# Kernel tuning notes

Hardware: AMD Instinct MI355X
Metric: run time of the kernel (lower is better)

## Reference

```python
import jax, jax.numpy as jnp
import numpy as np

N = 256    # num_nodes = 2*K*R
K = 16     # num_cluster (after reflection pairing)
R = 8      # ratio = size of each original cluster
IN = 32
OUT = 32
BS = 32


def setup_inputs() -> dict:
    key = jax.random.key(0)
    k1, k2, k3, k4 = jax.random.split(key, 4)
    x = jax.random.normal(k1, (BS, N, IN), dtype=jnp.float32)
    w_diag = jax.random.uniform(k2, (IN * OUT, K), dtype=jnp.float32)           # torch.rand
    w_off = jax.random.uniform(k3, (IN * OUT, K, 2 * K), dtype=jnp.float32)     # torch.rand
    stdv = 1.0 / np.sqrt(OUT)
    b1 = jax.random.uniform(k4, (OUT,), minval=-stdv, maxval=stdv, dtype=jnp.float32)
    perm = np.random.default_rng(0).permutation(N)   # flatten_ids of shuffled clusters
    permute_ids = jnp.asarray(perm, dtype=jnp.int32)
    inv_permute = jnp.asarray(np.argsort(perm), dtype=jnp.int32)
    return {"x": x, "w_diag": w_diag, "w_off": w_off, "b1": b1,
            "permute_ids": permute_ids, "inv_permute": inv_permute}


def _build_W(w_diag, w_off):
    # Faithful to: kron(tie_weights(w_off), ones(R,R))/N + kron(diag_embed(repeat_interleave(w_diag,2)), eye(R))
    C = w_diag.shape[0]            # in*out channels
    width = 2 * K
    # tie_weights: interleave original rows with pair-swapped-column rows
    swap = np.arange(width).reshape(-1, 2)[:, ::-1].reshape(-1)      # [1,0,3,2,...]
    tied = jnp.stack([w_off, w_off[:, :, swap]], axis=2).reshape(C, width, width)
    # kron with ones(R,R) == repeat each entry R times along both node axes
    W3 = jnp.repeat(jnp.repeat(tied, R, axis=1), R, axis=2) / N      # (C, N, N)
    # kron(diag_embed(.), eye(R)) == add per-node diagonal, constant within cluster
    wd_full = jnp.repeat(jnp.repeat(w_diag, 2, axis=1), R, axis=1)   # (C, N)
    di = jnp.arange(N)
    W3 = W3.at[:, di, di].add(wd_full)
    # rearrange '(o i) j k -> (o j) (i k)'
    return W3.reshape(OUT, IN, N, N).transpose(0, 2, 1, 3).reshape(OUT * N, IN * N)


def reference(x, w_diag, w_off, b1, permute_ids, inv_permute):
    W = _build_W(w_diag, w_off)                       # (OUT*N, IN*N)
    xp = x[:, permute_ids, :]                         # (BS, N, IN) permuted
    xp = xp.transpose(0, 2, 1).reshape(BS, IN * N)    # feature-major flatten
    out = xp @ W.T                                    # (BS, OUT*N)
    out = out.reshape(BS, OUT, N).transpose(0, 2, 1)  # (BS, N, OUT)
    out = out[:, inv_permute, :] + b1[None, None, :]
    return out
```

## Files before the change

kernel.cpp:

```cpp
#include <hip/hip_runtime.h>

#define N_   256
#define IN_  32
#define OUT_ 32
#define BS_  32

__global__ __launch_bounds__(256) void k_yz(const float* __restrict__ x,
                                            const int* __restrict__ perm,
                                            const float* __restrict__ w_off,
                                            float* __restrict__ ws_z) {
    const int t = threadIdx.x;
    const int b = blockIdx.x;
    const int o  = b & 31;
    const int sg = b >> 5;
    const int u  = t & 15;
    const int i4 = (t >> 4) & 7;
    const int sh = t >> 7;

    __shared__ int   perm_s[256];
    __shared__ float y_lds[4 * 32 * 32];
    __shared__ float part[128][8];

    perm_s[t] = perm[t];

    float4 wv[4][8];
    const float* wbase = w_off + ((o * 32 + i4 * 4) * 16 + u) * 32;
#pragma unroll
    for (int di = 0; di < 4; ++di)
#pragma unroll
        for (int q4 = 0; q4 < 8; ++q4)
            wv[di][q4] = *(const float4*)(wbase + di * 512 + q4 * 4);

    __syncthreads();

    {
        const int i  = t & 31;
        const int qb = t >> 5;
#pragma unroll
        for (int sl = 0; sl < 4; ++sl) {
            const float* xs = x + (sg * 4 + sl) * (N_ * IN_);
#pragma unroll
            for (int k = 0; k < 4; ++k) {
                const int q = qb * 4 + k;
                float sum = 0.f;
#pragma unroll
                for (int j = 0; j < 8; ++j)
                    sum += xs[perm_s[8 * q + j] * IN_ + i];
                y_lds[sl * 1024 + q * 32 + i] = sum;
            }
        }
    }
    __syncthreads();

#define WEL(di, qq) (((const float*)&wv[di][(qq) >> 2])[(qq) & 3])

    float accs[2][2];
#pragma unroll
    for (int dsi = 0; dsi < 2; ++dsi) {
        const float* yb = y_lds + (sh * 2 + dsi) * 1024 + i4 * 4;
        float a0 = 0.f, a1 = 0.f;
#pragma unroll
        for (int q = 0; q < 32; ++q) {
            const float4 yv = *(const float4*)(yb + q * 32);
            const int q1 = q ^ 1;
            a0 += WEL(0, q)  * yv.x + WEL(1, q)  * yv.y + WEL(2, q)  * yv.z + WEL(3, q)  * yv.w;
            a1 += WEL(0, q1) * yv.x + WEL(1, q1) * yv.y + WEL(2, q1) * yv.z + WEL(3, q1) * yv.w;
        }
        accs[dsi][0] = a0;
        accs[dsi][1] = a1;
    }
#undef WEL

#pragma unroll
    for (int dsi = 0; dsi < 2; ++dsi)
#pragma unroll
        for (int p = 0; p < 2; ++p) {
            const int slot = ((sh * 2 + dsi) * 16 + u) * 2 + p;
            part[slot][i4] = accs[dsi][p];
        }
    __syncthreads();

    if (t < 128) {
        float sum = 0.f;
#pragma unroll
        for (int j = 0; j < 8; ++j) sum += part[t][j];
        const int s_local = t >> 5;
        const int uu = (t >> 1) & 15;
        const int pp = t & 1;
        const int s = sg * 4 + s_local;
        ws_z[((s * 32 + o) * 16 + uu) * 2 + pp] = sum * (1.0f / 256.0f);
    }
}

__global__ __launch_bounds__(256) void k_out(const float* __restrict__ x,
                                             const int* __restrict__ perm,
                                             const float* __restrict__ w_diag,
                                             const float* __restrict__ b1,
                                             const float* __restrict__ ws_z,
                                             float* __restrict__ out) {
    const int t = threadIdx.x;
    const int b = blockIdx.x;
    const int s = b >> 3;
    const int ac = b & 7;

    __shared__ float xrow[32 * 32];
    __shared__ float wdt[2][32 * 36];
    __shared__ float z_lds[1024];
    __shared__ int perm_lds[32];

    if (t < 32) perm_lds[t] = perm[ac * 32 + t];

    ((float4*)z_lds)[t] = ((const float4*)(ws_z + s * 1024))[t];

    {
        const int o = t >> 3;
        const int ii = (t & 7) * 4;
#pragma unroll
        for (int uu = 0; uu < 2; ++uu)
#pragma unroll
            for (int d = 0; d < 4; ++d)
                wdt[uu][o * 36 + ii + d] = w_diag[(o * 32 + ii + d) * 16 + ac * 2 + uu];
    }
    {
        const int r = t >> 3;
        const int col = (t & 7) * 4;
        const int rowp = perm[ac * 32 + r];
        const float4 v = *(const float4*)(x + (s * N_ + rowp) * IN_ + col);
        *(float4*)&xrow[r * 32 + col] = v;
    }
    __syncthreads();

    const int o = t & 31;
    const int rg = t >> 5;
    const int u_sel = rg >> 2;
    const int p = (rg >> 1) & 1;
    const int u = ac * 2 + u_sel;

    float4 wreg[8];
#pragma unroll
    for (int ii = 0; ii < 8; ++ii)
        wreg[ii] = *(const float4*)&wdt[u_sel][o * 36 + ii * 4];

    const float base = b1[o] + z_lds[(o * 16 + u) * 2 + p];

#pragma unroll
    for (int dr = 0; dr < 4; ++dr) {
        const int r = rg * 4 + dr;
        const float4* xr = (const float4*)&xrow[r * 32];
        float acc = base;
#pragma unroll
        for (int ii = 0; ii < 8; ++ii) {
            const float4 xv = xr[ii];
            const float4 wv = wreg[ii];
            acc += xv.x * wv.x + xv.y * wv.y + xv.z * wv.z + xv.w * wv.w;
        }
        out[(s * N_ + perm_lds[r]) * OUT_ + o] = acc;
    }
}

extern "C" void kernel_launch(void* const* d_in, const int* in_sizes, int n_in,
                              void* d_out, int out_size, void* d_ws, size_t ws_size,
                              hipStream_t stream) {
    const float* x      = (const float*)d_in[0];
    const float* w_diag = (const float*)d_in[1];
    const float* w_off  = (const float*)d_in[2];
    const float* b1     = (const float*)d_in[3];
    const int*   perm   = (const int*)d_in[4];

    float* out = (float*)d_out;
    float* ws_z = (float*)d_ws;

    k_yz<<<256, 256, 0, stream>>>(x, perm, w_off, ws_z);
    k_out<<<256, 256, 0, stream>>>(x, perm, w_diag, b1, ws_z, out);
}
```

Before: 75.51 us.

## Fuse cluster-sum and output kernels into one per-sample, per-cluster-block kernel

Merges the two kernels into a single kernel where each block owns one sample and a block of 32 nodes. It computes the cluster sums and the off-diagonal contribution locally instead of staging z through workspace memory. This removes a kernel launch and the global round trip, but each block now recomputes the cluster sums for its sample (8x redundancy). It also loads w_off tiles for only its two clusters, in two sequential register loads.

```diff
diff --git a/kernel.cpp b/kernel.cpp
--- a/kernel.cpp
+++ b/kernel.cpp
@@ -5,26 +5,31 @@
 #define OUT_ 32
 #define BS_  32
 
-__global__ __launch_bounds__(256) void k_yz(const float* __restrict__ x,
-                                            const int* __restrict__ perm,
-                                            const float* __restrict__ w_off,
-                                            float* __restrict__ ws_z) {
+__global__ __launch_bounds__(256) void k_fused(const float* __restrict__ x,
+                                               const int* __restrict__ perm,
+                                               const float* __restrict__ w_diag,
+                                               const float* __restrict__ w_off,
+                                               const float* __restrict__ b1,
+                                               float* __restrict__ out) {
     const int t = threadIdx.x;
     const int b = blockIdx.x;
-    const int o  = b & 31;
-    const int sg = b >> 5;
-    const int u  = t & 15;
-    const int i4 = (t >> 4) & 7;
-    const int sh = t >> 7;
+    const int s  = b >> 3;
+    const int ac = b & 7;
 
     __shared__ int   perm_s[256];
-    __shared__ float y_lds[4 * 32 * 32];
-    __shared__ float part[128][8];
+    __shared__ float y_lds[1024];
+    __shared__ float part[128][9];
+    __shared__ float z_lds[128];
+    __shared__ float xrow[1024];
+    __shared__ float wdt[2][32 * 36];
 
     perm_s[t] = perm[t];
 
+    const int o  = t & 31;
+    const int i4 = t >> 5;
+
+    const float* wbase = w_off + ((o * 32 + i4 * 4) * 16 + 2 * ac) * 32;
     float4 wv[4][8];
-    const float* wbase = w_off + ((o * 32 + i4 * 4) * 16 + u) * 32;
 #pragma unroll
     for (int di = 0; di < 4; ++di)
 #pragma unroll
@@ -34,30 +39,46 @@
     __syncthreads();
 
     {
-        const int i  = t & 31;
-        const int qb = t >> 5;
+        const float* xs = x + s * (N_ * IN_);
 #pragma unroll
-        for (int sl = 0; sl < 4; ++sl) {
-            const float* xs = x + (sg * 4 + sl) * (N_ * IN_);
+        for (int k = 0; k < 4; ++k) {
+            const int q = i4 * 4 + k;
+            float sum = 0.f;
 #pragma unroll
-            for (int k = 0; k < 4; ++k) {
-                const int q = qb * 4 + k;
-                float sum = 0.f;
+            for (int j = 0; j < 8; ++j)
+                sum += xs[perm_s[8 * q + j] * IN_ + o];
+            y_lds[q * 32 + o] = sum;
+        }
+    }
+    {
+        const int r = t >> 3;
+        const int col = (t & 7) * 4;
+        const float4 v = *(const float4*)(x + (s * N_ + perm_s[ac * 32 + r]) * IN_ + col);
+        *(float4*)&xrow[r * 32 + col] = v;
+    }
+    {
+        const int oo = t >> 3;
+        const int ii = (t & 7) * 4;
 #pragma unroll
-                for (int j = 0; j < 8; ++j)
-                    sum += xs[perm_s[8 * q + j] * IN_ + i];
-                y_lds[sl * 1024 + q * 32 + i] = sum;
-            }
-        }
+        for (int uu = 0; uu < 2; ++uu)
+#pragma unroll
+            for (int d = 0; d < 4; ++d)
+                wdt[uu][oo * 36 + ii + d] = w_diag[(oo * 32 + ii + d) * 16 + ac * 2 + uu];
     }
     __syncthreads();
 
 #define WEL(di, qq) (((const float*)&wv[di][(qq) >> 2])[(qq) & 3])
 
-    float accs[2][2];
+    const float* yb = y_lds + i4 * 4;
 #pragma unroll
-    for (int dsi = 0; dsi < 2; ++dsi) {
-        const float* yb = y_lds + (sh * 2 + dsi) * 1024 + i4 * 4;
+    for (int u_l = 0; u_l < 2; ++u_l) {
+        if (u_l == 1) {
+#pragma unroll
+            for (int di = 0; di < 4; ++di)
+#pragma unroll
+                for (int q4 = 0; q4 < 8; ++q4)
+                    wv[di][q4] = *(const float4*)(wbase + di * 512 + 32 + q4 * 4);
+        }
         float a0 = 0.f, a1 = 0.f;
 #pragma unroll
         for (int q = 0; q < 32; ++q) {
@@ -66,82 +87,34 @@
             a0 += WEL(0, q)  * yv.x + WEL(1, q)  * yv.y + WEL(2, q)  * yv.z + WEL(3, q)  * yv.w;
             a1 += WEL(0, q1) * yv.x + WEL(1, q1) * yv.y + WEL(2, q1) * yv.z + WEL(3, q1) * yv.w;
         }
-        accs[dsi][0] = a0;
-        accs[dsi][1] = a1;
+        part[u_l * 64 + o * 2 + 0][i4] = a0;
+        part[u_l * 64 + o * 2 + 1][i4] = a1;
     }
 #undef WEL
 
-#pragma unroll
-    for (int dsi = 0; dsi < 2; ++dsi)
-#pragma unroll
-        for (int p = 0; p < 2; ++p) {
-            const int slot = ((sh * 2 + dsi) * 16 + u) * 2 + p;
-            part[slot][i4] = accs[dsi][p];
-        }
     __syncthreads();
 
     if (t < 128) {
         float sum = 0.f;
 #pragma unroll
         for (int j = 0; j < 8; ++j) sum += part[t][j];
-        const int s_local = t >> 5;
-        const int uu = (t >> 1) & 15;
+        const int u_l = t >> 6;
+        const int oo = (t >> 1) & 31;
         const int pp = t & 1;
-        const int s = sg * 4 + s_local;
-        ws_z[((s * 32 + o) * 16 + uu) * 2 + pp] = sum * (1.0f / 256.0f);
-    }
-}
-
-__global__ __launch_bounds__(256) void k_out(const float* __restrict__ x,
-                                             const int* __restrict__ perm,
-                                             const float* __restrict__ w_diag,
-                                             const float* __restrict__ b1,
-                                             const float* __restrict__ ws_z,
-                                             float* __restrict__ out) {
-    const int t = threadIdx.x;
-    const int b = blockIdx.x;
-    const int s = b >> 3;
-    const int ac = b & 7;
-
-    __shared__ float xrow[32 * 32];
-    __shared__ float wdt[2][32 * 36];
-    __shared__ float z_lds[1024];
-    __shared__ int perm_lds[32];
-
-    if (t < 32) perm_lds[t] = perm[ac * 32 + t];
-
-    ((float4*)z_lds)[t] = ((const float4*)(ws_z + s * 1024))[t];
-
-    {
-        const int o = t >> 3;
-        const int ii = (t & 7) * 4;
-#pragma unroll
-        for (int uu = 0; uu < 2; ++uu)
-#pragma unroll
-            for (int d = 0; d < 4; ++d)
-                wdt[uu][o * 36 + ii + d] = w_diag[(o * 32 + ii + d) * 16 + ac * 2 + uu];
-    }
-    {
-        const int r = t >> 3;
-        const int col = (t & 7) * 4;
-        const int rowp = perm[ac * 32 + r];
-        const float4 v = *(const float4*)(x + (s * N_ + rowp) * IN_ + col);
-        *(float4*)&xrow[r * 32 + col] = v;
+        z_lds[oo * 4 + u_l * 2 + pp] = sum * (1.0f / 256.0f);
     }
     __syncthreads();
 
-    const int o = t & 31;
     const int rg = t >> 5;
     const int u_sel = rg >> 2;
     const int p = (rg >> 1) & 1;
-    const int u = ac * 2 + u_sel;
 
     float4 wreg[8];
 #pragma unroll
     for (int ii = 0; ii < 8; ++ii)
         wreg[ii] = *(const float4*)&wdt[u_sel][o * 36 + ii * 4];
 
-    const float base = b1[o] + z_lds[(o * 16 + u) * 2 + p];
+    const float base = b1[o] + z_lds[o * 4 + u_sel * 2 + p];
 
 #pragma unroll
     for (int dr = 0; dr < 4; ++dr) {
@@ -151,10 +124,10 @@
 #pragma unroll
         for (int ii = 0; ii < 8; ++ii) {
             const float4 xv = xr[ii];
-            const float4 wv = wreg[ii];
-            acc += xv.x * wv.x + xv.y * wv.y + xv.z * wv.z + xv.w * wv.w;
+            const float4 wvv = wreg[ii];
+            acc += xv.x * wvv.x + xv.y * wvv.y + xv.z * wvv.z + xv.w * wvv.w;
         }
-        out[(s * N_ + perm_lds[r]) * OUT_ + o] = acc;
+        out[(s * N_ + perm_s[ac * 32 + r]) * OUT_ + o] = acc;
     }
 }
 
@@ -166,10 +139,7 @@
     const float* w_off  = (const float*)d_in[2];
     const float* b1     = (const float*)d_in[3];
     const int*   perm   = (const int*)d_in[4];
+    float* out = (float*)d_out;
 
-    float* out = (float*)d_out;
-    float* ws_z = (float*)d_ws;
-
-    k_yz<<<256, 256, 0, stream>>>(x, perm, w_off, ws_z);
-    k_out<<<256, 256, 0, stream>>>(x, perm, w_diag, b1, ws_z, out);
+    k_fused<<<256, 256, 0, stream>>>(x, perm, w_diag, w_off, b1, out);
 }
```

Measured after the change: 78.25 us. +3.6%, slower.
